# Kernel optimization log

Hardware: AMD Instinct MI355X
Metric: run time of the kernel (lower is better)

## Reference

```python
import jax, jax.numpy as jnp
import numpy as np

B, C, Q, E = 32, 1024, 64, 256  # batch, max_context_len, max_question_len, embedding_size
FE = 4 * E                      # final_encoding_size (self_attention=False)


def setup_inputs() -> dict:
    key = jax.random.key(0)
    ks = jax.random.split(key, 7)
    return {
        "context": jax.random.normal(ks[0], (B, C, E), dtype=jnp.float32),
        "question": jax.random.normal(ks[1], (B, Q, E), dtype=jnp.float32),
        "context_mask": jnp.ones((B, C), dtype=jnp.float32),
        "w_question": jax.random.normal(ks[2], (E,), dtype=jnp.float32),
        "w_context": jax.random.normal(ks[3], (E,), dtype=jnp.float32),
        "w_multiple": jax.random.normal(ks[4], (E,), dtype=jnp.float32),
        "final_W": jax.random.normal(ks[5], (FE, FE), dtype=jnp.float32) * (1.0 / np.sqrt(FE)),
        "final_b": jnp.zeros((FE,), dtype=jnp.float32),
    }


def reference(context, question, context_mask, w_question, w_context, w_multiple, final_W, final_b):
    # Trilinear similarity: s[b,c,q] = <w_q, q_q> + <w_c, c_c> + <w_m, c_c * q_q>
    q_weighted = question @ w_question                 # (B, Q)
    ctx_weighted = context @ w_context                 # (B, C)
    # (question.unsqueeze(1) * context.unsqueeze(2)) @ w_multiple, computed
    # without materializing the (B, C, Q, E) intermediate:
    mult = jnp.einsum('bce,bqe->bcq', context * w_multiple, question)  # (B, C, Q)
    similarity = ctx_weighted[:, :, None] + q_weighted[:, None, :] + mult  # (B, C, Q)

    # Context-to-query attention (softmax over question dim)
    c2q_att = jnp.einsum('bcq,bqe->bce', jax.nn.softmax(similarity, axis=2), question)

    # Query-to-context attention (softmax over context dim of row-max scores)
    q2c_weights = jax.nn.softmax(jnp.max(similarity, axis=2), axis=1)   # (B, C)
    q2c_att = jnp.einsum('bc,bce->be', q2c_weights, context)            # (B, E)

    attended = jnp.concatenate(
        [context, c2q_att, context * c2q_att, context * q2c_att[:, None, :]],
        axis=2)                                                          # (B, C, 4E)

    # MaskedLinear: affine map, output rows zeroed where context_mask == 0
    out = (attended @ final_W.T + final_b) * context_mask[:, :, None]    # (B, C, 4E)
    return out
```

## Files before the change

kernel.cpp:

```cpp
#include <hip/hip_runtime.h>

#define BB 32
#define CC 1024
#define QQ 64
#define EE 256
#define FE 1024
#define MM (BB*CC)

typedef __bf16 bf16_t;
typedef bf16_t bf16x8 __attribute__((ext_vector_type(8)));
typedef float f32x4 __attribute__((ext_vector_type(4)));
typedef unsigned short u16x8 __attribute__((ext_vector_type(8)));

__device__ __forceinline__ unsigned short f2bf(float f) {
  unsigned u = __float_as_uint(f);
  u += 0x7fffu + ((u >> 16) & 1u);
  return (unsigned short)(u >> 16);
}
__device__ __forceinline__ float bf2f(unsigned short u) {
  return __uint_as_float(((unsigned)u) << 16);
}

__device__ __forceinline__ void gload_lds16(const void* g, void* l) {
  __builtin_amdgcn_global_load_lds(
      (const __attribute__((address_space(1))) unsigned int*)g,
      (__attribute__((address_space(3))) unsigned int*)l, 16, 0, 0);
}

__global__ void k_prep(const float* __restrict__ question, const float* __restrict__ w_question,
                       float* __restrict__ qw,
                       const float* __restrict__ W, unsigned short* __restrict__ Wb) {
  int bx = blockIdx.x;
  if (bx < 512) {
    int gid = bx * 256 + threadIdx.x;
    int row = gid >> 6;
    int lane = gid & 63;
    const float4 q = *(const float4*)(question + (size_t)row * EE + lane * 4);
    const float4 wq = *(const float4*)(w_question + lane * 4);
    float d = q.x*wq.x + q.y*wq.y + q.z*wq.z + q.w*wq.w;
    d += __shfl_xor(d, 1);  d += __shfl_xor(d, 2);  d += __shfl_xor(d, 4);
    d += __shfl_xor(d, 8);  d += __shfl_xor(d, 16); d += __shfl_xor(d, 32);
    if (lane == 0) qw[row] = d;
  } else {
    int i = ((bx - 512) * 256 + threadIdx.x) * 4;
    float4 v = *(const float4*)(W + i);
    ushort4 o; o.x = f2bf(v.x); o.y = f2bf(v.y); o.z = f2bf(v.z); o.w = f2bf(v.w);
    *(ushort4*)(Wb + i) = o;
  }
}

#define DOT4(acc, A, Bv) acc += A.x*Bv.x + A.y*Bv.y + A.z*Bv.z + A.w*Bv.w

__launch_bounds__(256)
__global__ void k_simpv(const float* __restrict__ ctx, const float* __restrict__ question,
                        const float* __restrict__ qw_g, const float* __restrict__ w_context,
                        const float* __restrict__ w_multiple,
                        float* __restrict__ rowmax, unsigned short* __restrict__ att) {
  __shared__ float qbuf[QQ * 132];
  __shared__ float ck[64][36];
  __shared__ unsigned short Pl[QQ][68];
  __shared__ float cwl[64];
  __shared__ float qwl[QQ];
  const int tid = threadIdx.x;
  const int b = blockIdx.y;
  const int c0 = blockIdx.x * 64;
  const int tx = tid & 15, ty = tid >> 4;

  const float* qb = question + (size_t)b * (QQ * EE);
  if (tid < QQ) qwl[tid] = qw_g[b * QQ + tid];

  const int cr = tid >> 3, er = (tid & 7) * 4;
  const float* crow0 = ctx + ((size_t)(b * CC + c0 + cr)) * EE;
  const float* crow1 = crow0 + 32 * EE;
  unsigned short* arow0 = att + ((size_t)(b * CC + c0 + cr)) * FE;
  unsigned short* arow1 = arow0 + (size_t)32 * FE;
  float s[4][4] = {{0.f}};
  float cp0 = 0.f, cp1 = 0.f;

  for (int h = 0; h < 2; ++h) {
    if (h) __syncthreads();
    for (int idx = tid * 4; idx < QQ * 128; idx += 1024) {
      int row = idx >> 7, col = idx & 127;
      *(float4*)&qbuf[row * 132 + col] = *(const float4*)(qb + (size_t)row * EE + h * 128 + col);
    }
    for (int eo2 = 0; eo2 < 128; eo2 += 32) {
      const int eo = h * 128 + eo2;
      float4 cv0 = *(const float4*)(crow0 + eo + er);
      float4 cv1 = *(const float4*)(crow1 + eo + er);
      float4 wc = *(const float4*)(w_context + eo + er);
      float4 wm = *(const float4*)(w_multiple + eo + er);
      cp0 += cv0.x*wc.x + cv0.y*wc.y + cv0.z*wc.z + cv0.w*wc.w;
      cp1 += cv1.x*wc.x + cv1.y*wc.y + cv1.z*wc.z + cv1.w*wc.w;
      ushort4 u0, u1;
      u0.x = f2bf(cv0.x); u0.y = f2bf(cv0.y); u0.z = f2bf(cv0.z); u0.w = f2bf(cv0.w);
      u1.x = f2bf(cv1.x); u1.y = f2bf(cv1.y); u1.z = f2bf(cv1.z); u1.w = f2bf(cv1.w);
      *(ushort4*)(arow0 + eo + er) = u0;
      *(ushort4*)(arow1 + eo + er) = u1;
      __syncthreads();
      float4 m0, m1;
      m0.x = cv0.x*wm.x; m0.y = cv0.y*wm.y; m0.z = cv0.z*wm.z; m0.w = cv0.w*wm.w;
      m1.x = cv1.x*wm.x; m1.y = cv1.y*wm.y; m1.z = cv1.z*wm.z; m1.w = cv1.w*wm.w;
      *(float4*)&ck[cr][er] = m0;
      *(float4*)&ck[cr + 32][er] = m1;
      __syncthreads();
#pragma unroll
      for (int ee = 0; ee < 32; ee += 4) {
        float4 a0 = *(const float4*)&ck[ty +  0][ee];
        float4 a1 = *(const float4*)&ck[ty + 16][ee];
        float4 a2 = *(const float4*)&ck[ty + 32][ee];
        float4 a3 = *(const float4*)&ck[ty + 48][ee];
        float4 b0 = *(const float4*)&qbuf[(tx +  0) * 132 + eo2 + ee];
        float4 b1 = *(const float4*)&qbuf[(tx + 16) * 132 + eo2 + ee];
        float4 b2 = *(const float4*)&qbuf[(tx + 32) * 132 + eo2 + ee];
        float4 b3 = *(const float4*)&qbuf[(tx + 48) * 132 + eo2 + ee];
        DOT4(s[0][0], a0, b0); DOT4(s[0][1], a0, b1); DOT4(s[0][2], a0, b2); DOT4(s[0][3], a0, b3);
        DOT4(s[1][0], a1, b0); DOT4(s[1][1], a1, b1); DOT4(s[1][2], a1, b2); DOT4(s[1][3], a1, b3);
        DOT4(s[2][0], a2, b0); DOT4(s[2][1], a2, b1); DOT4(s[2][2], a2, b2); DOT4(s[2][3], a2, b3);
        DOT4(s[3][0], a3, b0); DOT4(s[3][1], a3, b1); DOT4(s[3][2], a3, b2); DOT4(s[3][3], a3, b3);
      }
    }
  }
  cp0 += __shfl_xor(cp0, 1); cp0 += __shfl_xor(cp0, 2); cp0 += __shfl_xor(cp0, 4);
  cp1 += __shfl_xor(cp1, 1); cp1 += __shfl_xor(cp1, 2); cp1 += __shfl_xor(cp1, 4);
  if ((tid & 7) == 0) { cwl[cr] = cp0; cwl[cr + 32] = cp1; }
  __syncthreads();

#pragma unroll
  for (int i = 0; i < 4; ++i) {
    int c = ty + 16 * i;
    float cw = cwl[c];
    float f[4], mx = -1e30f;
#pragma unroll
    for (int j = 0; j < 4; ++j) {
      f[j] = s[i][j] + cw + qwl[tx + 16 * j];
      mx = fmaxf(mx, f[j]);
    }
    mx = fmaxf(mx, __shfl_xor(mx, 1));
    mx = fmaxf(mx, __shfl_xor(mx, 2));
    mx = fmaxf(mx, __shfl_xor(mx, 4));
    mx = fmaxf(mx, __shfl_xor(mx, 8));
    float sum = 0.f;
#pragma unroll
    for (int j = 0; j < 4; ++j) { f[j] = expf(f[j] - mx); sum += f[j]; }
    sum += __shfl_xor(sum, 1);
    sum += __shfl_xor(sum, 2);
    sum += __shfl_xor(sum, 4);
    sum += __shfl_xor(sum, 8);
    float inv = 1.f / sum;
    if (tx == 0) rowmax[(size_t)b * CC + c0 + c] = mx;
#pragma unroll
    for (int j = 0; j < 4; ++j) Pl[tx + 16 * j][c] = f2bf(f[j] * inv);
  }
  __syncthreads();

  for (int ep = 0; ep < EE; ep += 64) {
    if (ep) __syncthreads();
    {
      int q = tid >> 2, e16 = (tid & 3) * 16;
      const float* src = qb + (size_t)q * EE + ep + e16;
      *(float4*)&qbuf[q * 68 + e16 +  0] = *(const float4*)(src);
      *(float4*)&qbuf[q * 68 + e16 +  4] = *(const float4*)(src + 4);
      *(float4*)&qbuf[q * 68 + e16 +  8] = *(const float4*)(src + 8);
      *(float4*)&qbuf[q * 68 + e16 + 12] = *(const float4*)(src + 12);
    }
    __syncthreads();
    float s2[4][4] = {{0.f}};
#pragma unroll 8
    for (int q = 0; q < QQ; ++q) {
      float a0 = bf2f(Pl[q][ty +  0]);
      float a1 = bf2f(Pl[q][ty + 16]);
      float a2 = bf2f(Pl[q][ty + 32]);
      float a3 = bf2f(Pl[q][ty + 48]);
      float4 bv = *(const float4*)&qbuf[q * 68 + tx * 4];
      s2[0][0] += a0 * bv.x; s2[0][1] += a0 * bv.y; s2[0][2] += a0 * bv.z; s2[0][3] += a0 * bv.w;
      s2[1][0] += a1 * bv.x; s2[1][1] += a1 * bv.y; s2[1][2] += a1 * bv.z; s2[1][3] += a1 * bv.w;
      s2[2][0] += a2 * bv.x; s2[2][1] += a2 * bv.y; s2[2][2] += a2 * bv.z; s2[2][3] += a2 * bv.w;
      s2[3][0] += a3 * bv.x; s2[3][1] += a3 * bv.y; s2[3][2] += a3 * bv.z; s2[3][3] += a3 * bv.w;
    }
#pragma unroll
    for (int i = 0; i < 4; ++i) {
      int c = ty + 16 * i;
      size_t row = (size_t)(b * CC + c0 + c);
      unsigned short* arow = att + row * (size_t)FE;
      ushort4 cu = *(const ushort4*)(arow + ep + tx * 4);
      float cx = bf2f(cu.x), cy = bf2f(cu.y), cz = bf2f(cu.z), cw = bf2f(cu.w);
      ushort4 o1, o2;
      o1.x = f2bf(s2[i][0]);       o1.y = f2bf(s2[i][1]);       o1.z = f2bf(s2[i][2]);       o1.w = f2bf(s2[i][3]);
      o2.x = f2bf(cx * s2[i][0]);  o2.y = f2bf(cy * s2[i][1]);  o2.z = f2bf(cz * s2[i][2]);  o2.w = f2bf(cw * s2[i][3]);
      *(ushort4*)(arow + 1 * EE + ep + tx * 4) = o1;
      *(ushort4*)(arow + 2 * EE + ep + tx * 4) = o2;
    }
  }
}

__global__ void k_q2c_softmax(const float* __restrict__ rowmax, float* __restrict__ q2cw) {
  int b = blockIdx.x, tid = threadIdx.x;
  __shared__ float rbuf[4], sbuf[4];
  float4 v = *(const float4*)(rowmax + (size_t)b * CC + tid * 4);
  float m = fmaxf(fmaxf(v.x, v.y), fmaxf(v.z, v.w));
  for (int off = 1; off < 64; off <<= 1) m = fmaxf(m, __shfl_xor(m, off));
  int wv = tid >> 6;
  if ((tid & 63) == 0) rbuf[wv] = m;
  __syncthreads();
  m = fmaxf(fmaxf(rbuf[0], rbuf[1]), fmaxf(rbuf[2], rbuf[3]));
  float e0 = expf(v.x - m), e1 = expf(v.y - m), e2 = expf(v.z - m), e3 = expf(v.w - m);
  float sum = e0 + e1 + e2 + e3;
  for (int off = 1; off < 64; off <<= 1) sum += __shfl_xor(sum, off);
  if ((tid & 63) == 0) sbuf[wv] = sum;
  __syncthreads();
  sum = sbuf[0] + sbuf[1] + sbuf[2] + sbuf[3];
  float inv = 1.f / sum;
  float4 o; o.x = e0 * inv; o.y = e1 * inv; o.z = e2 * inv; o.w = e3 * inv;
  *(float4*)(q2cw + (size_t)b * CC + tid * 4) = o;
}

__global__ void k_q2c_part(const unsigned short* __restrict__ att, const float* __restrict__ w,
                           float* __restrict__ part) {
  int b = blockIdx.y, ch = blockIdx.x;
  int e = threadIdx.x;
  const unsigned short* base = att + ((size_t)(b * CC + ch * 128)) * FE + e;
  const float* wp = w + b * CC + ch * 128;
  float acc = 0.f;
#pragma unroll 4
  for (int c = 0; c < 128; ++c) acc += wp[c] * bf2f(base[(size_t)c * FE]);
  part[(b * 8 + ch) * EE + e] = acc;
}

__global__ void k_wmod(const unsigned short* __restrict__ Wb, const float* __restrict__ part,
                       unsigned short* __restrict__ att) {
  __shared__ float q2cl[EE];
  const int b = blockIdx.y;
  const int t = threadIdx.x;
  {
    float a = 0.f;
#pragma unroll
    for (int ch = 0; ch < 8; ++ch) a += part[(b * 8 + ch) * EE + t];
    q2cl[t] = a;
  }
  __syncthreads();
  const int n = blockIdx.x * 8 + (t >> 5);
  const int e = (t & 31) * 8;
  u16x8 w1 = *(const u16x8*)(Wb + (size_t)n * FE + e);
  u16x8 w4 = *(const u16x8*)(Wb + (size_t)n * FE + 768 + e);
  float4 g0 = *(const float4*)&q2cl[e];
  float4 g1 = *(const float4*)&q2cl[e + 4];
  u16x8 o;
  o[0] = f2bf(bf2f(w1[0]) + bf2f(w4[0]) * g0.x);
  o[1] = f2bf(bf2f(w1[1]) + bf2f(w4[1]) * g0.y);
  o[2] = f2bf(bf2f(w1[2]) + bf2f(w4[2]) * g0.z);
  o[3] = f2bf(bf2f(w1[3]) + bf2f(w4[3]) * g0.w);
  o[4] = f2bf(bf2f(w1[4]) + bf2f(w4[4]) * g1.x);
  o[5] = f2bf(bf2f(w1[5]) + bf2f(w4[5]) * g1.y);
  o[6] = f2bf(bf2f(w1[6]) + bf2f(w4[6]) * g1.z);
  o[7] = f2bf(bf2f(w1[7]) + bf2f(w4[7]) * g1.w);
  *(u16x8*)(att + ((size_t)(b * CC + n)) * FE + 768 + e) = o;
}

__launch_bounds__(256, 3)
__global__ void k_gemm(const unsigned short* __restrict__ A, const unsigned short* __restrict__ Bw,
                       const float* __restrict__ bias, const float* __restrict__ mask,
                       float* __restrict__ out) {
  __shared__ bf16_t As[128][32];
  __shared__ bf16_t Bs[128][32];
  const int tid = threadIdx.x;
  const int lane = tid & 63;
  const int wave = tid >> 6;
  const int wr = wave >> 1, wc = wave & 1;

  const int bid = blockIdx.x;
  const int wg = (bid & 7) * 256 + (bid >> 3);
  const int bcol = (wg & 7) * 128;
  const int brow = (wg >> 3) * 128;
  const int bb = brow >> 10;

  const int r = lane & 15, kg = lane >> 4;
  const int rk = (kg ^ ((r >> 2) & 3)) * 8;

  const int srow = tid >> 2;
  const int sgr = tid & 3;
  const int ssw = (sgr ^ ((srow >> 2) & 3)) * 8;
  const unsigned short* gA0 = A + (size_t)(brow + srow) * FE + ssw;
  const unsigned short* gA1 = gA0 + (size_t)64 * FE;
  const unsigned short* gB0 = Bw + (size_t)(bcol + srow) * FE + ssw;
  const unsigned short* gB1 = gB0 + (size_t)64 * FE;
  const unsigned short* gW0 = A + (size_t)(bb * CC + bcol + srow) * FE + 768 + ssw;
  const unsigned short* gW1 = gW0 + (size_t)64 * FE;
  bf16_t* dA0 = &As[srow][sgr * 8];
  bf16_t* dA1 = dA0 + 64 * 32;
  bf16_t* dB0 = &Bs[srow][sgr * 8];
  bf16_t* dB1 = dB0 + 64 * 32;

  f32x4 acc[4][4] = {};

  for (int k0 = 0; k0 < 768; k0 += 32) {
    gload_lds16(gA0 + k0, dA0);
    gload_lds16(gA1 + k0, dA1);
    if (k0 < 256) {
      gload_lds16(gW0 + k0, dB0);
      gload_lds16(gW1 + k0, dB1);
    } else {
      gload_lds16(gB0 + k0, dB0);
      gload_lds16(gB1 + k0, dB1);
    }
    __syncthreads();
    bf16x8 fa[4], fb[4];
#pragma unroll
    for (int m = 0; m < 4; ++m) fa[m] = *(const bf16x8*)&As[wr * 64 + m * 16 + r][rk];
#pragma unroll
    for (int n = 0; n < 4; ++n) fb[n] = *(const bf16x8*)&Bs[wc * 64 + n * 16 + r][rk];
#pragma unroll
    for (int m = 0; m < 4; ++m)
#pragma unroll
      for (int n = 0; n < 4; ++n)
        acc[m][n] = __builtin_amdgcn_mfma_f32_16x16x32_bf16(fa[m], fb[n], acc[m][n], 0, 0, 0);
    __syncthreads();
  }

#pragma unroll
  for (int m = 0; m < 4; ++m) {
#pragma unroll
    for (int n = 0; n < 4; ++n) {
#pragma unroll
      for (int reg = 0; reg < 4; ++reg) {
        int row = brow + wr * 64 + m * 16 + kg * 4 + reg;
        int col = bcol + wc * 64 + n * 16 + r;
        out[(size_t)row * FE + col] = (acc[m][n][reg] + bias[col]) * mask[row];
      }
    }
  }
}

extern "C" void kernel_launch(void* const* d_in, const int* in_sizes, int n_in,
                              void* d_out, int out_size, void* d_ws, size_t ws_size,
                              hipStream_t stream) {
  const float* ctx  = (const float*)d_in[0];
  const float* ques = (const float*)d_in[1];
  const float* mask = (const float*)d_in[2];
  const float* w_q  = (const float*)d_in[3];
  const float* w_c  = (const float*)d_in[4];
  const float* w_m  = (const float*)d_in[5];
  const float* fW   = (const float*)d_in[6];
  const float* fb   = (const float*)d_in[7];
  float* out = (float*)d_out;

  char* ws = (char*)d_ws;
  float* qw     = (float*)(ws);
  float* rowmax = (float*)(ws + 8192);
  float* q2cw   = (float*)(ws + 139264);
  float* part   = (float*)(ws + 270336);
  unsigned short* attended = (unsigned short*)(ws + 1048576);
  unsigned short* Wb       = (unsigned short*)(ws + 68157440);

  k_prep<<<1536, 256, 0, stream>>>(ques, w_q, qw, fW, Wb);
  k_simpv<<<dim3(16, 32), 256, 0, stream>>>(ctx, ques, qw, w_c, w_m, rowmax, attended);
  k_q2c_softmax<<<32, 256, 0, stream>>>(rowmax, q2cw);
  k_q2c_part<<<dim3(8, 32), 256, 0, stream>>>(attended, q2cw, part);
  k_wmod<<<dim3(128, 32), 256, 0, stream>>>(Wb, part, attended);
  k_gemm<<<2048, 256, 0, stream>>>(attended, Wb, fb, mask, out);
}
```

Before: 159.1 us.

## Double GEMM K-tile, stage epilogue through LDS, fuse q2c softmax into partial sum

The GEMM K-step grows from 32 to 64 with an 8-way XOR swizzle, which halves the number of barrier pairs per tile. The epilogue now stages accumulators through padded LDS so each thread can write coalesced float4 output rows instead of scattered scalar stores. The q2c softmax kernel is folded into k_q2c_part, where every block recomputes the per-batch max and sum, removing one launch at the cost of redundant reductions. The larger LDS footprint (32KB) may reduce occupancy relative to the launch bound of 3 blocks per CU.

```diff
diff --git a/kernel.cpp b/kernel.cpp
--- a/kernel.cpp
+++ b/kernel.cpp
@@ -193,37 +193,29 @@
   }
 }
 
-__global__ void k_q2c_softmax(const float* __restrict__ rowmax, float* __restrict__ q2cw) {
-  int b = blockIdx.x, tid = threadIdx.x;
-  __shared__ float rbuf[4], sbuf[4];
-  float4 v = *(const float4*)(rowmax + (size_t)b * CC + tid * 4);
+__global__ void k_q2c_part(const unsigned short* __restrict__ att, const float* __restrict__ rowmax,
+                           float* __restrict__ part) {
+  __shared__ float red[8];
+  __shared__ float wl[128];
+  const int b = blockIdx.y, ch = blockIdx.x, t = threadIdx.x;
+  float4 v = *(const float4*)(rowmax + (size_t)b * CC + t * 4);
   float m = fmaxf(fmaxf(v.x, v.y), fmaxf(v.z, v.w));
   for (int off = 1; off < 64; off <<= 1) m = fmaxf(m, __shfl_xor(m, off));
-  int wv = tid >> 6;
-  if ((tid & 63) == 0) rbuf[wv] = m;
-  __syncthreads();
-  m = fmaxf(fmaxf(rbuf[0], rbuf[1]), fmaxf(rbuf[2], rbuf[3]));
-  float e0 = expf(v.x - m), e1 = expf(v.y - m), e2 = expf(v.z - m), e3 = expf(v.w - m);
-  float sum = e0 + e1 + e2 + e3;
-  for (int off = 1; off < 64; off <<= 1) sum += __shfl_xor(sum, off);
-  if ((tid & 63) == 0) sbuf[wv] = sum;
-  __syncthreads();
-  sum = sbuf[0] + sbuf[1] + sbuf[2] + sbuf[3];
-  float inv = 1.f / sum;
-  float4 o; o.x = e0 * inv; o.y = e1 * inv; o.z = e2 * inv; o.w = e3 * inv;
-  *(float4*)(q2cw + (size_t)b * CC + tid * 4) = o;
-}
-
-__global__ void k_q2c_part(const unsigned short* __restrict__ att, const float* __restrict__ w,
-                           float* __restrict__ part) {
-  int b = blockIdx.y, ch = blockIdx.x;
-  int e = threadIdx.x;
-  const unsigned short* base = att + ((size_t)(b * CC + ch * 128)) * FE + e;
-  const float* wp = w + b * CC + ch * 128;
+  if ((t & 63) == 0) red[t >> 6] = m;
+  __syncthreads();
+  m = fmaxf(fmaxf(red[0], red[1]), fmaxf(red[2], red[3]));
+  float s = expf(v.x - m) + expf(v.y - m) + expf(v.z - m) + expf(v.w - m);
+  for (int off = 1; off < 64; off <<= 1) s += __shfl_xor(s, off);
+  if ((t & 63) == 0) red[4 + (t >> 6)] = s;
+  __syncthreads();
+  float inv = 1.f / (red[4] + red[5] + red[6] + red[7]);
+  if (t < 128) wl[t] = expf(rowmax[(size_t)b * CC + ch * 128 + t] - m) * inv;
+  __syncthreads();
+  const unsigned short* base = att + ((size_t)(b * CC + ch * 128)) * FE + t;
   float acc = 0.f;
 #pragma unroll 4
-  for (int c = 0; c < 128; ++c) acc += wp[c] * bf2f(base[(size_t)c * FE]);
-  part[(b * 8 + ch) * EE + e] = acc;
+  for (int c = 0; c < 128; ++c) acc += wl[c] * bf2f(base[(size_t)c * FE]);
+  part[(b * 8 + ch) * EE + t] = acc;
 }
 
 __global__ void k_wmod(const unsigned short* __restrict__ Wb, const float* __restrict__ part,
@@ -260,8 +252,10 @@
 __global__ void k_gemm(const unsigned short* __restrict__ A, const unsigned short* __restrict__ Bw,
                        const float* __restrict__ bias, const float* __restrict__ mask,
                        float* __restrict__ out) {
-  __shared__ bf16_t As[128][32];
-  __shared__ bf16_t Bs[128][32];
+  __shared__ __align__(16) unsigned char LDSBUF[32768];
+  bf16_t* As = (bf16_t*)LDSBUF;
+  bf16_t* Bs = As + 128 * 64;
+  float* sm = (float*)LDSBUF;
   const int tid = threadIdx.x;
   const int lane = tid & 63;
   const int wave = tid >> 6;
@@ -274,58 +268,79 @@
   const int bb = brow >> 10;
 
   const int r = lane & 15, kg = lane >> 4;
-  const int rk = (kg ^ ((r >> 2) & 3)) * 8;
-
-  const int srow = tid >> 2;
-  const int sgr = tid & 3;
-  const int ssw = (sgr ^ ((srow >> 2) & 3)) * 8;
-  const unsigned short* gA0 = A + (size_t)(brow + srow) * FE + ssw;
-  const unsigned short* gA1 = gA0 + (size_t)64 * FE;
-  const unsigned short* gB0 = Bw + (size_t)(bcol + srow) * FE + ssw;
-  const unsigned short* gB1 = gB0 + (size_t)64 * FE;
-  const unsigned short* gW0 = A + (size_t)(bb * CC + bcol + srow) * FE + 768 + ssw;
-  const unsigned short* gW1 = gW0 + (size_t)64 * FE;
-  bf16_t* dA0 = &As[srow][sgr * 8];
-  bf16_t* dA1 = dA0 + 64 * 32;
-  bf16_t* dB0 = &Bs[srow][sgr * 8];
-  bf16_t* dB1 = dB0 + 64 * 32;
+
+  const int srow = tid >> 3;
+  const int ssw = ((tid & 7) ^ (srow & 7)) * 8;
+  const unsigned short* gA = A  + (size_t)(brow + srow) * FE + ssw;
+  const unsigned short* gB = Bw + (size_t)(bcol + srow) * FE + ssw;
+  const unsigned short* gW = A  + (size_t)(bb * CC + bcol + srow) * FE + 768 + ssw;
+  bf16_t* dA = As + tid * 8;
+  bf16_t* dB = Bs + tid * 8;
 
   f32x4 acc[4][4] = {};
 
-  for (int k0 = 0; k0 < 768; k0 += 32) {
-    gload_lds16(gA0 + k0, dA0);
-    gload_lds16(gA1 + k0, dA1);
+  for (int k0 = 0; k0 < 768; k0 += 64) {
+#pragma unroll
+    for (int i = 0; i < 4; ++i)
+      gload_lds16(gA + (size_t)(i * 32) * FE + k0, dA + i * 2048);
     if (k0 < 256) {
-      gload_lds16(gW0 + k0, dB0);
-      gload_lds16(gW1 + k0, dB1);
+#pragma unroll
+      for (int i = 0; i < 4; ++i)
+        gload_lds16(gW + (size_t)(i * 32) * FE + k0, dB + i * 2048);
     } else {
-      gload_lds16(gB0 + k0, dB0);
-      gload_lds16(gB1 + k0, dB1);
+#pragma unroll
+      for (int i = 0; i < 4; ++i)
+        gload_lds16(gB + (size_t)(i * 32) * FE + k0, dB + i * 2048);
     }
     __syncthreads();
-    bf16x8 fa[4], fb[4];
-#pragma unroll
-    for (int m = 0; m < 4; ++m) fa[m] = *(const bf16x8*)&As[wr * 64 + m * 16 + r][rk];
-#pragma unroll
-    for (int n = 0; n < 4; ++n) fb[n] = *(const bf16x8*)&Bs[wc * 64 + n * 16 + r][rk];
-#pragma unroll
-    for (int m = 0; m < 4; ++m)
-#pragma unroll
-      for (int n = 0; n < 4; ++n)
-        acc[m][n] = __builtin_amdgcn_mfma_f32_16x16x32_bf16(fa[m], fb[n], acc[m][n], 0, 0, 0);
+
+    bf16x8 fa[4][2], fb[4][2];
+#pragma unroll
+    for (int m = 0; m < 4; ++m) {
+      const int row_ = wr * 64 + m * 16 + r;
+#pragma unroll
+      for (int ks = 0; ks < 2; ++ks)
+        fa[m][ks] = *(const bf16x8*)(As + row_ * 64 + (((ks * 4 + kg) ^ (row_ & 7)) * 8));
+    }
+#pragma unroll
+    for (int n = 0; n < 4; ++n) {
+      const int row_ = wc * 64 + n * 16 + r;
+#pragma unroll
+      for (int ks = 0; ks < 2; ++ks)
+        fb[n][ks] = *(const bf16x8*)(Bs + row_ * 64 + (((ks * 4 + kg) ^ (row_ & 7)) * 8));
+    }
+#pragma unroll
+    for (int ks = 0; ks < 2; ++ks)
+#pragma unroll
+      for (int m = 0; m < 4; ++m)
+#pragma unroll
+        for (int n = 0; n < 4; ++n)
+          acc[m][n] = __builtin_amdgcn_mfma_f32_16x16x32_bf16(fa[m][ks], fb[n][ks], acc[m][n], 0, 0, 0);
     __syncthreads();
   }
 
+  const int lrow = tid >> 3;
+  const int co = (tid & 7) * 4;
 #pragma unroll
   for (int m = 0; m < 4; ++m) {
-#pragma unroll
-    for (int n = 0; n < 4; ++n) {
-#pragma unroll
-      for (int reg = 0; reg < 4; ++reg) {
-        int row = brow + wr * 64 + m * 16 + kg * 4 + reg;
-        int col = bcol + wc * 64 + n * 16 + r;
-        out[(size_t)row * FE + col] = (acc[m][n][reg] + bias[col]) * mask[row];
-      }
+    if (m) __syncthreads();
+#pragma unroll
+    for (int n = 0; n < 4; ++n)
+#pragma unroll
+      for (int reg = 0; reg < 4; ++reg)
+        sm[(wr * 16 + kg * 4 + reg) * 133 + wc * 64 + n * 16 + r] = acc[m][n][reg];
+    __syncthreads();
+    const int grow = brow + (lrow >> 4) * 64 + m * 16 + (lrow & 15);
+    const float mk = mask[grow];
+    float* orow = out + (size_t)grow * FE + bcol;
+#pragma unroll
+    for (int j = 0; j < 4; ++j) {
+      const int c = co + j * 32;
+      float4 v = *(float4*)&sm[lrow * 133 + c];
+      float4 bz = *(const float4*)(bias + bcol + c);
+      float4 o; o.x = (v.x + bz.x) * mk; o.y = (v.y + bz.y) * mk;
+      o.z = (v.z + bz.z) * mk; o.w = (v.w + bz.w) * mk;
+      *(float4*)(orow + c) = o;
     }
   }
 }
@@ -346,15 +361,13 @@
   char* ws = (char*)d_ws;
   float* qw     = (float*)(ws);
   float* rowmax = (float*)(ws + 8192);
-  float* q2cw   = (float*)(ws + 139264);
-  float* part   = (float*)(ws + 270336);
+  float* part   = (float*)(ws + 139264);
   unsigned short* attended = (unsigned short*)(ws + 1048576);
   unsigned short* Wb       = (unsigned short*)(ws + 68157440);
 
   k_prep<<<1536, 256, 0, stream>>>(ques, w_q, qw, fW, Wb);
   k_simpv<<<dim3(16, 32), 256, 0, stream>>>(ctx, ques, qw, w_c, w_m, rowmax, attended);
-  k_q2c_softmax<<<32, 256, 0, stream>>>(rowmax, q2cw);
-  k_q2c_part<<<dim3(8, 32), 256, 0, stream>>>(attended, q2cw, part);
+  k_q2c_part<<<dim3(8, 32), 256, 0, stream>>>(attended, rowmax, part);
   k_wmod<<<dim3(128, 32), 256, 0, stream>>>(Wb, part, attended);
   k_gemm<<<2048, 256, 0, stream>>>(attended, Wb, fb, mask, out);
 }
```

New measurement: 151.6 us, median of 3. 1.05x faster.
